# Kernel tuning notes

Measured on AMD Instinct MI355X. Metric: run time of the kernel, lower is better.

The kernel has to match this reference:

```python
import jax, jax.numpy as jnp
import numpy as np

B, N, C_IN, C_OUT, K = 16, 16384, 128, 128, 9


def setup_inputs() -> dict:
    key = jax.random.key(0)
    ks = jax.random.split(key, 7)
    x = jax.random.normal(ks[0], (B, N, C_IN), dtype=jnp.float32)
    indices = jax.random.randint(ks[1], (N, K), 0, N, dtype=jnp.int32)
    # P initialized near identity (as in the torch module) plus small noise
    P = jnp.eye(K, dtype=jnp.float32)[None].repeat(N, axis=0) \
        + 0.02 * jax.random.normal(ks[2], (N, K, K), dtype=jnp.float32)
    W_conv = jax.random.normal(ks[3], (C_OUT, K * C_IN), dtype=jnp.float32) * (1.0 / np.sqrt(K * C_IN))
    b_conv = jax.random.normal(ks[4], (C_OUT,), dtype=jnp.float32) * 0.01
    W_skip = jax.random.normal(ks[5], (C_OUT, C_IN), dtype=jnp.float32) * (1.0 / np.sqrt(C_IN))
    b_skip = jax.random.normal(ks[6], (C_OUT,), dtype=jnp.float32) * 0.01
    return {"x": x, "indices": indices, "P": P, "W_conv": W_conv,
            "b_conv": b_conv, "W_skip": W_skip, "b_skip": b_skip}


def reference(x, indices, P, W_conv, b_conv, W_skip, b_skip):
    b, n, c = x.shape
    k = P.shape[-1]
    # pad node axis with k zero rows (matches x_padded in torch module)
    x_pad = jnp.concatenate([x, jnp.zeros((b, k, c), dtype=x.dtype)], axis=1)
    # gather k neighbours per node: (b, n, k, c)
    nbr = jnp.take(x_pad, indices, axis=1)
    # per-node kxk permutation/mixing matmul: P (n,k,k) @ nbr (b,n,k,c)
    perm = jnp.einsum('nkj,bnjc->bnkc', P, nbr)
    flat = jax.nn.elu(perm.reshape(b, n, k * c))
    z = jax.nn.elu(jnp.einsum('bnf,of->bno', flat, W_conv) + b_conv)
    # skip connection
    z = jnp.einsum('bnc,oc->bno', x, W_skip) + b_skip + z
    return z
```

## Files before the change

kernel.cpp:

```cpp
#include <hip/hip_runtime.h>
#include <hip/hip_fp16.h>
#include <math.h>

#define B_ 16
#define N_ 16384
#define C_ 128
#define K_ 9
#define FCONV 1152
#define G_ 2
#define FPAD 1160
#define LDS_BYTES (G_ * B_ * FPAD * 2)

typedef _Float16 half8 __attribute__((ext_vector_type(8)));
typedef float floatx4 __attribute__((ext_vector_type(4)));

__device__ __forceinline__ float elu_f(float v) {
    return v > 0.f ? v : (__expf(v) - 1.f);
}

__global__ void build_wfrag(const float* __restrict__ Wc, const float* __restrict__ Ws,
                            _Float16* __restrict__ WcF, _Float16* __restrict__ WsF) {
    const int i = blockIdx.x * 256 + threadIdx.x;
    if (i < 8 * 36 * 64 * 8) {
        const int j = i & 7, lane = (i >> 3) & 63;
        const int rest = i >> 9;
        const int kc = rest % 36, ot = rest / 36;
        WcF[i] = (_Float16)Wc[(size_t)(ot * 16 + (lane & 15)) * FCONV + kc * 32 + (lane >> 4) * 8 + j];
    }
    if (i < 8 * 4 * 64 * 8) {
        const int j = i & 7, lane = (i >> 3) & 63;
        const int rest = i >> 9;
        const int kc = rest & 3, ot = rest >> 2;
        WsF[i] = (_Float16)Ws[(size_t)(ot * 16 + (lane & 15)) * C_ + kc * 32 + (lane >> 4) * 8 + j];
    }
}

template <bool WF16>
__global__ __launch_bounds__(256) void paiconv_mfma(
    const float* __restrict__ x,
    const int*   __restrict__ idx,
    const float* __restrict__ P,
    const void*  __restrict__ WcP,
    const float* __restrict__ bc,
    const void*  __restrict__ WsP,
    const float* __restrict__ bs,
    float*       __restrict__ out)
{
    extern __shared__ _Float16 flat_s[];
    __shared__ float P_s[G_ * 81];
    __shared__ int   idx_s[G_ * K_];

    const int tid = threadIdx.x;
    const int n0  = blockIdx.x * G_;

    if (tid < G_ * 81) {
        const int g = tid / 81, t = tid - g * 81;
        P_s[tid] = P[(size_t)(n0 + g) * 81 + t];
    }
    if (tid < G_ * K_) {
        const int g = tid / K_, j = tid - g * K_;
        idx_s[tid] = idx[(size_t)(n0 + g) * K_ + j];
    }
    __syncthreads();

    {
        const int c = tid & (C_ - 1);
        const int h = tid >> 7;
        for (int g = 0; g < G_; ++g) {
            int id[K_];
            #pragma unroll
            for (int j = 0; j < K_; ++j) id[j] = idx_s[g * K_ + j];
            const float* Pg = &P_s[g * 81];
            _Float16* fg = &flat_s[g * (B_ * FPAD)];

            float v[8][K_];
            #pragma unroll
            for (int i = 0; i < 8; ++i) {
                const int m = h * 8 + i;
                const float* xb = x + (size_t)m * (N_ * C_) + c;
                #pragma unroll
                for (int j = 0; j < K_; ++j)
                    v[i][j] = ((unsigned)id[j] < (unsigned)N_) ? xb[(size_t)id[j] * C_] : 0.f;
            }
            #pragma unroll
            for (int k = 0; k < K_; ++k) {
                float pr[K_];
                #pragma unroll
                for (int j = 0; j < K_; ++j) pr[j] = Pg[k * K_ + j];
                #pragma unroll
                for (int i = 0; i < 8; ++i) {
                    float s = 0.f;
                    #pragma unroll
                    for (int j = 0; j < K_; ++j) s = fmaf(pr[j], v[i][j], s);
                    fg[(h * 8 + i) * FPAD + k * C_ + c] = (_Float16)elu_f(s);
                }
            }
        }
    }
    __syncthreads();

    const int w    = tid >> 6;
    const int lane = tid & 63;
    const int col  = lane & 15;
    const int quad = lane >> 4;
    const int o0   = w * 32;

    floatx4 accC[G_][2], accS[G_][2];
    #pragma unroll
    for (int g = 0; g < G_; ++g)
        #pragma unroll
        for (int t = 0; t < 2; ++t) {
            accC[g][t] = (floatx4){0.f, 0.f, 0.f, 0.f};
            accS[g][t] = (floatx4){0.f, 0.f, 0.f, 0.f};
        }

    for (int k0 = 0; k0 < FCONV; k0 += 32) {
        half8 a[G_];
        #pragma unroll
        for (int g = 0; g < G_; ++g)
            a[g] = *(const half8*)&flat_s[g * (B_ * FPAD) + col * FPAD + k0 + quad * 8];
        #pragma unroll
        for (int t = 0; t < 2; ++t) {
            half8 b;
            if (WF16) {
                b = ((const half8*)WcP)[((w * 2 + t) * 36 + (k0 >> 5)) * 64 + lane];
            } else {
                const float* p = (const float*)WcP + (size_t)(o0 + t * 16 + col) * FCONV + k0 + quad * 8;
                const float4 w0 = *(const float4*)p;
                const float4 w1 = *(const float4*)(p + 4);
                b = (half8){(_Float16)w0.x, (_Float16)w0.y, (_Float16)w0.z, (_Float16)w0.w,
                            (_Float16)w1.x, (_Float16)w1.y, (_Float16)w1.z, (_Float16)w1.w};
            }
            #pragma unroll
            for (int g = 0; g < G_; ++g)
                accC[g][t] = __builtin_amdgcn_mfma_f32_16x16x32_f16(a[g], b, accC[g][t], 0, 0, 0);
        }
    }

    for (int k0 = 0; k0 < C_; k0 += 32) {
        half8 a[G_];
        #pragma unroll
        for (int g = 0; g < G_; ++g) {
            const float* p = x + (size_t)col * (N_ * C_) + (size_t)(n0 + g) * C_ + k0 + quad * 8;
            const float4 x0 = *(const float4*)p;
            const float4 x1 = *(const float4*)(p + 4);
            a[g] = (half8){(_Float16)x0.x, (_Float16)x0.y, (_Float16)x0.z, (_Float16)x0.w,
                           (_Float16)x1.x, (_Float16)x1.y, (_Float16)x1.z, (_Float16)x1.w};
        }
        #pragma unroll
        for (int t = 0; t < 2; ++t) {
            half8 b;
            if (WF16) {
                b = ((const half8*)WsP)[((w * 2 + t) * 4 + (k0 >> 5)) * 64 + lane];
            } else {
                const float* p = (const float*)WsP + (size_t)(o0 + t * 16 + col) * C_ + k0 + quad * 8;
                const float4 w0 = *(const float4*)p;
                const float4 w1 = *(const float4*)(p + 4);
                b = (half8){(_Float16)w0.x, (_Float16)w0.y, (_Float16)w0.z, (_Float16)w0.w,
                            (_Float16)w1.x, (_Float16)w1.y, (_Float16)w1.z, (_Float16)w1.w};
            }
            #pragma unroll
            for (int g = 0; g < G_; ++g)
                accS[g][t] = __builtin_amdgcn_mfma_f32_16x16x32_f16(a[g], b, accS[g][t], 0, 0, 0);
        }
    }

    float bcv[2], bsv[2];
    #pragma unroll
    for (int t = 0; t < 2; ++t) {
        bcv[t] = bc[o0 + t * 16 + col];
        bsv[t] = bs[o0 + t * 16 + col];
    }
    #pragma unroll
    for (int g = 0; g < G_; ++g) {
        const int n = n0 + g;
        #pragma unroll
        for (int t = 0; t < 2; ++t) {
            const int o = o0 + t * 16 + col;
            #pragma unroll
            for (int r = 0; r < 4; ++r) {
                const int m = quad * 4 + r;
                const float z = elu_f(accC[g][t][r] + bcv[t]);
                out[((size_t)m * N_ + n) * C_ + o] = z + accS[g][t][r] + bsv[t];
            }
        }
    }
}

extern "C" void kernel_launch(void* const* d_in, const int* in_sizes, int n_in,
                              void* d_out, int out_size, void* d_ws, size_t ws_size,
                              hipStream_t stream) {
    const float* x   = (const float*)d_in[0];
    const int*   idx = (const int*)  d_in[1];
    const float* P   = (const float*)d_in[2];
    const float* Wc  = (const float*)d_in[3];
    const float* bc  = (const float*)d_in[4];
    const float* Ws  = (const float*)d_in[5];
    const float* bs  = (const float*)d_in[6];
    float* out = (float*)d_out;

    const size_t wc_halfs = (size_t)8 * 36 * 64 * 8;
    const size_t ws_halfs = (size_t)8 * 4 * 64 * 8;
    const size_t need = (wc_halfs + ws_halfs) * sizeof(_Float16);

    if (ws_size >= need) {
        _Float16* WcF = (_Float16*)d_ws;
        _Float16* WsF = WcF + wc_halfs;
        build_wfrag<<<dim3(576), dim3(256), 0, stream>>>(Wc, Ws, WcF, WsF);
        hipFuncSetAttribute((const void*)paiconv_mfma<true>,
                            hipFuncAttributeMaxDynamicSharedMemorySize, LDS_BYTES);
        paiconv_mfma<true><<<dim3(N_ / G_), dim3(256), LDS_BYTES, stream>>>(
            x, idx, P, WcF, bc, WsF, bs, out);
    } else {
        hipFuncSetAttribute((const void*)paiconv_mfma<false>,
                            hipFuncAttributeMaxDynamicSharedMemorySize, LDS_BYTES);
        paiconv_mfma<false><<<dim3(N_ / G_), dim3(256), LDS_BYTES, stream>>>(
            x, idx, P, Wc, bc, Ws, bs, out);
    }
}
```

Measured before the change: 622.5 us.

## Quadruple block size to 1024 threads and split MFMA work per wave

The block grows from 256 to 1024 threads, so each thread gathers 2 batches instead of 8. In the MFMA phase each of the 16 waves handles one node and one 16-wide output tile instead of two nodes by two tiles. The P and idx shared-memory staging is removed and each thread reads them from global memory directly, and output stores become nontemporal. The aim is more parallelism and less register pressure per thread, in exchange for larger blocks, launch_bounds(1024,8) register caps, and redundant global reads of P and idx.

New measurement: 598.5 us. 1.04x faster.

```diff
diff --git a/kernel.cpp b/kernel.cpp
--- a/kernel.cpp
+++ b/kernel.cpp
@@ -36,7 +36,7 @@
 }
 
 template <bool WF16>
-__global__ __launch_bounds__(256) void paiconv_mfma(
+__global__ __launch_bounds__(1024, 8) void paiconv_mfma(
     const float* __restrict__ x,
     const int*   __restrict__ idx,
     const float* __restrict__ P,
@@ -47,52 +47,43 @@
     float*       __restrict__ out)
 {
     extern __shared__ _Float16 flat_s[];
-    __shared__ float P_s[G_ * 81];
-    __shared__ int   idx_s[G_ * K_];
 
     const int tid = threadIdx.x;
     const int n0  = blockIdx.x * G_;
 
-    if (tid < G_ * 81) {
-        const int g = tid / 81, t = tid - g * 81;
-        P_s[tid] = P[(size_t)(n0 + g) * 81 + t];
-    }
-    if (tid < G_ * K_) {
-        const int g = tid / K_, j = tid - g * K_;
-        idx_s[tid] = idx[(size_t)(n0 + g) * K_ + j];
-    }
-    __syncthreads();
-
     {
-        const int c = tid & (C_ - 1);
-        const int h = tid >> 7;
+        const int c  = tid & (C_ - 1);
+        const int bg = tid >> 7;
+        #pragma unroll
         for (int g = 0; g < G_; ++g) {
+            const int n = n0 + g;
             int id[K_];
             #pragma unroll
-            for (int j = 0; j < K_; ++j) id[j] = idx_s[g * K_ + j];
-            const float* Pg = &P_s[g * 81];
-            _Float16* fg = &flat_s[g * (B_ * FPAD)];
+            for (int j = 0; j < K_; ++j) id[j] = idx[(size_t)n * K_ + j];
 
-            float v[8][K_];
+            float v[2][K_];
             #pragma unroll
-            for (int i = 0; i < 8; ++i) {
-                const int m = h * 8 + i;
+            for (int i = 0; i < 2; ++i) {
+                const int m = bg * 2 + i;
                 const float* xb = x + (size_t)m * (N_ * C_) + c;
                 #pragma unroll
                 for (int j = 0; j < K_; ++j)
                     v[i][j] = ((unsigned)id[j] < (unsigned)N_) ? xb[(size_t)id[j] * C_] : 0.f;
             }
+
+            _Float16* fg = &flat_s[g * (B_ * FPAD)];
+            const float* Pn = P + (size_t)n * 81;
             #pragma unroll
             for (int k = 0; k < K_; ++k) {
                 float pr[K_];
                 #pragma unroll
-                for (int j = 0; j < K_; ++j) pr[j] = Pg[k * K_ + j];
+                for (int j = 0; j < K_; ++j) pr[j] = Pn[k * K_ + j];
                 #pragma unroll
-                for (int i = 0; i < 8; ++i) {
+                for (int i = 0; i < 2; ++i) {
                     float s = 0.f;
                     #pragma unroll
                     for (int j = 0; j < K_; ++j) s = fmaf(pr[j], v[i][j], s);
-                    fg[(h * 8 + i) * FPAD + k * C_ + c] = (_Float16)elu_f(s);
+                    fg[(bg * 2 + i) * FPAD + k * C_ + c] = (_Float16)elu_f(s);
                 }
             }
         }
@@ -103,87 +94,57 @@
     const int lane = tid & 63;
     const int col  = lane & 15;
     const int quad = lane >> 4;
-    const int o0   = w * 32;
+    const int g    = w & 1;
+    const int ot   = w >> 1;
+    const int o0   = ot * 16;
+    const int n    = n0 + g;
 
-    floatx4 accC[G_][2], accS[G_][2];
-    #pragma unroll
-    for (int g = 0; g < G_; ++g)
-        #pragma unroll
-        for (int t = 0; t < 2; ++t) {
-            accC[g][t] = (floatx4){0.f, 0.f, 0.f, 0.f};
-            accS[g][t] = (floatx4){0.f, 0.f, 0.f, 0.f};
+    floatx4 accC = (floatx4){0.f, 0.f, 0.f, 0.f};
+    floatx4 accS = (floatx4){0.f, 0.f, 0.f, 0.f};
+
+    for (int k0 = 0; k0 < C_; k0 += 32) {
+        const float* p = x + (size_t)col * (N_ * C_) + (size_t)n * C_ + k0 + quad * 8;
+        const float4 x0 = *(const float4*)p;
+        const float4 x1 = *(const float4*)(p + 4);
+        half8 a = (half8){(_Float16)x0.x, (_Float16)x0.y, (_Float16)x0.z, (_Float16)x0.w,
+                          (_Float16)x1.x, (_Float16)x1.y, (_Float16)x1.z, (_Float16)x1.w};
+        half8 b;
+        if (WF16) {
+            b = ((const half8*)WsP)[(ot * 4 + (k0 >> 5)) * 64 + lane];
+        } else {
+            const float* q = (const float*)WsP + (size_t)(o0 + col) * C_ + k0 + quad * 8;
+            const float4 w0 = *(const float4*)q;
+            const float4 w1 = *(const float4*)(q + 4);
+            b = (half8){(_Float16)w0.x, (_Float16)w0.y, (_Float16)w0.z, (_Float16)w0.w,
+                        (_Float16)w1.x, (_Float16)w1.y, (_Float16)w1.z, (_Float16)w1.w};
         }
-
-    for (int k0 = 0; k0 < FCONV; k0 += 32) {
-        half8 a[G_];
-        #pragma unroll
-        for (int g = 0; g < G_; ++g)
-            a[g] = *(const half8*)&flat_s[g * (B_ * FPAD) + col * FPAD + k0 + quad * 8];
-        #pragma unroll
-        for (int t = 0; t < 2; ++t) {
-            half8 b;
-            if (WF16) {
-                b = ((const half8*)WcP)[((w * 2 + t) * 36 + (k0 >> 5)) * 64 + lane];
-            } else {
-                const float* p = (const float*)WcP + (size_t)(o0 + t * 16 + col) * FCONV + k0 + quad * 8;
-                const float4 w0 = *(const float4*)p;
-                const float4 w1 = *(const float4*)(p + 4);
-                b = (half8){(_Float16)w0.x, (_Float16)w0.y, (_Float16)w0.z, (_Float16)w0.w,
-                            (_Float16)w1.x, (_Float16)w1.y, (_Float16)w1.z, (_Float16)w1.w};
-            }
-            #pragma unroll
-            for (int g = 0; g < G_; ++g)
-                accC[g][t] = __builtin_amdgcn_mfma_f32_16x16x32_f16(a[g], b, accC[g][t], 0, 0, 0);
-        }
+        accS = __builtin_amdgcn_mfma_f32_16x16x32_f16(a, b, accS, 0, 0, 0);
     }
 
-    for (int k0 = 0; k0 < C_; k0 += 32) {
-        half8 a[G_];
-        #pragma unroll
-        for (int g = 0; g < G_; ++g) {
-            const float* p = x + (size_t)col * (N_ * C_) + (size_t)(n0 + g) * C_ + k0 + quad * 8;
-            const float4 x0 = *(const float4*)p;
-            const float4 x1 = *(const float4*)(p + 4);
-            a[g] = (half8){(_Float16)x0.x, (_Float16)x0.y, (_Float16)x0.z, (_Float16)x0.w,
-                           (_Float16)x1.x, (_Float16)x1.y, (_Float16)x1.z, (_Float16)x1.w};
+    const _Float16* fg = &flat_s[g * (B_ * FPAD) + col * FPAD];
+    for (int k0 = 0; k0 < FCONV; k0 += 32) {
+        half8 a = *(const half8*)&fg[k0 + quad * 8];
+        half8 b;
+        if (WF16) {
+            b = ((const half8*)WcP)[(ot * 36 + (k0 >> 5)) * 64 + lane];
+        } else {
+            const float* q = (const float*)WcP + (size_t)(o0 + col) * FCONV + k0 + quad * 8;
+            const float4 w0 = *(const float4*)q;
+            const float4 w1 = *(const float4*)(q + 4);
+            b = (half8){(_Float16)w0.x, (_Float16)w0.y, (_Float16)w0.z, (_Float16)w0.w,
+                        (_Float16)w1.x, (_Float16)w1.y, (_Float16)w1.z, (_Float16)w1.w};
         }
-        #pragma unroll
-        for (int t = 0; t < 2; ++t) {
-            half8 b;
-            if (WF16) {
-                b = ((const half8*)WsP)[((w * 2 + t) * 4 + (k0 >> 5)) * 64 + lane];
-            } else {
-                const float* p = (const float*)WsP + (size_t)(o0 + t * 16 + col) * C_ + k0 + quad * 8;
-                const float4 w0 = *(const float4*)p;
-                const float4 w1 = *(const float4*)(p + 4);
-                b = (half8){(_Float16)w0.x, (_Float16)w0.y, (_Float16)w0.z, (_Float16)w0.w,
-                            (_Float16)w1.x, (_Float16)w1.y, (_Float16)w1.z, (_Float16)w1.w};
-            }
-            #pragma unroll
-            for (int g = 0; g < G_; ++g)
-                accS[g][t] = __builtin_amdgcn_mfma_f32_16x16x32_f16(a[g], b, accS[g][t], 0, 0, 0);
-        }
+        accC = __builtin_amdgcn_mfma_f32_16x16x32_f16(a, b, accC, 0, 0, 0);
     }
 
-    float bcv[2], bsv[2];
+    const float bcv = bc[o0 + col];
+    const float bsv = bs[o0 + col];
     #pragma unroll
-    for (int t = 0; t < 2; ++t) {
-        bcv[t] = bc[o0 + t * 16 + col];
-        bsv[t] = bs[o0 + t * 16 + col];
-    }
-    #pragma unroll
-    for (int g = 0; g < G_; ++g) {
-        const int n = n0 + g;
-        #pragma unroll
-        for (int t = 0; t < 2; ++t) {
-            const int o = o0 + t * 16 + col;
-            #pragma unroll
-            for (int r = 0; r < 4; ++r) {
-                const int m = quad * 4 + r;
-                const float z = elu_f(accC[g][t][r] + bcv[t]);
-                out[((size_t)m * N_ + n) * C_ + o] = z + accS[g][t][r] + bsv[t];
-            }
-        }
+    for (int r = 0; r < 4; ++r) {
+        const int m = quad * 4 + r;
+        const float z = elu_f(accC[r] + bcv);
+        __builtin_nontemporal_store(z + accS[r] + bsv,
+                                    &out[((size_t)m * N_ + n) * C_ + o0 + col]);
     }
 }
 
@@ -209,12 +170,12 @@
         build_wfrag<<<dim3(576), dim3(256), 0, stream>>>(Wc, Ws, WcF, WsF);
         hipFuncSetAttribute((const void*)paiconv_mfma<true>,
                             hipFuncAttributeMaxDynamicSharedMemorySize, LDS_BYTES);
-        paiconv_mfma<true><<<dim3(N_ / G_), dim3(256), LDS_BYTES, stream>>>(
+        paiconv_mfma<true><<<dim3(N_ / G_), dim3(1024), LDS_BYTES, stream>>>(
             x, idx, P, WcF, bc, WsF, bs, out);
     } else {
         hipFuncSetAttribute((const void*)paiconv_mfma<false>,
                             hipFuncAttributeMaxDynamicSharedMemorySize, LDS_BYTES);
-        paiconv_mfma<false><<<dim3(N_ / G_), dim3(256), LDS_BYTES, stream>>>(
+        paiconv_mfma<false><<<dim3(N_ / G_), dim3(1024), LDS_BYTES, stream>>>(
             x, idx, P, Wc, bc, Ws, bs, out);
     }
 }
```
